# Optimization experiments

Hardware: AMD Instinct MI355X
Metric: run time of the kernel (lower is better)

Reference implementation:

```python
import jax, jax.numpy as jnp
import numpy as np

L, B, T, S, W, H = 4, 2, 2048, 512, 512, 8  # layers, batch, n_ctx, cond units, width, heads
CH = W // H


def _ln(x, g, b):
    m = x.mean(-1, keepdims=True)
    v = ((x - m) ** 2).mean(-1, keepdims=True)
    return (x - m) * jax.lax.rsqrt(v + 1e-5) * g + b


def setup_inputs() -> dict:
    key = jax.random.key(0)
    ks = jax.random.split(key, 16)
    std = 0.25 * np.sqrt(1.0 / W)  # init_scale * sqrt(1/width), as in Transformer.__init__
    f32 = jnp.float32
    d = {
        "x": jax.random.normal(ks[0], (B, T, W), f32),
        "cond_k": jax.random.normal(ks[1], (B, S, W), f32),
        "cond_v": jax.random.normal(ks[2], (B, S, W), f32),
        # stacked per-layer params; weights stored [in, out] (torch Linear transposed)
        "qkv_w": jax.random.normal(ks[3], (L, W, 3 * W), f32) * std,
        "qkv_b": jnp.zeros((L, 3 * W), f32),
        "attn_proj_w": jax.random.normal(ks[4], (L, W, W), f32) * std,
        "attn_proj_b": jnp.zeros((L, W), f32),
        "cross_proj_w": jax.random.normal(ks[5], (L, W, W), f32) * std,
        "cross_proj_b": jnp.zeros((L, W), f32),
        "fc_w": jax.random.normal(ks[6], (L, W, 4 * W), f32) * std,
        "fc_b": jnp.zeros((L, 4 * W), f32),
        "mlp_proj_w": jax.random.normal(ks[7], (L, 4 * W, W), f32) * std,
        "mlp_proj_b": jnp.zeros((L, W), f32),
        "ln1_g": jnp.ones((L, W), f32), "ln1_b": jnp.zeros((L, W), f32),
        "ln3_g": jnp.ones((L, W), f32), "ln3_b": jnp.zeros((L, W), f32),
        "ln4_g": jnp.ones((L, W), f32), "ln4_b": jnp.zeros((L, W), f32),
    }
    return d


def reference(x, cond_k, cond_v, qkv_w, qkv_b, attn_proj_w, attn_proj_b,
              cross_proj_w, cross_proj_b, fc_w, fc_b, mlp_proj_w, mlp_proj_b,
              ln1_g, ln1_b, ln3_g, ln3_b, ln4_g, ln4_b):
    b, t, w = x.shape
    ch = w // H
    scale = 1.0 / np.sqrt(np.sqrt(ch))  # applied to both q and k, as in torch code
    kk = cond_k.reshape(b, -1, H, ch)
    vv = cond_v.reshape(b, -1, H, ch)
    n_layers = qkv_w.shape[0]
    for i in range(n_layers):
        # ---- self-attention ----
        h = _ln(x, ln1_g[i], ln1_b[i])
        qkv = (h @ qkv_w[i] + qkv_b[i]).reshape(b, t, H, 3 * ch)
        q, k, v = qkv[..., :ch], qkv[..., ch:2 * ch], qkv[..., 2 * ch:]
        wts = jnp.einsum('bthc,bshc->bhts', q * scale, k * scale)
        wts = jax.nn.softmax(wts.astype(jnp.float32), axis=-1).astype(wts.dtype)
        a = jnp.einsum('bhts,bshc->bthc', wts, v).reshape(b, t, w)
        x = x + a @ attn_proj_w[i] + attn_proj_b[i]
        # ---- cross-attention (q is ln_3(x) directly, no q projection) ----
        h = _ln(x, ln3_g[i], ln3_b[i])
        q = h.reshape(b, t, H, ch)
        wts = jnp.einsum('bthc,bshc->bhts', q * scale, kk * scale)
        wts = jax.nn.softmax(wts.astype(jnp.float32), axis=-1).astype(wts.dtype)
        a = jnp.einsum('bhts,bshc->bthc', wts, vv).reshape(b, t, w)
        x = x + a @ cross_proj_w[i] + cross_proj_b[i]
        # ---- MLP (exact erf GELU, as torch nn.GELU default) ----
        h = _ln(x, ln4_g[i], ln4_b[i])
        h = jax.nn.gelu(h @ fc_w[i] + fc_b[i], approximate=False)
        x = x + h @ mlp_proj_w[i] + mlp_proj_b[i]
    return x
```

## Files before the change

### kernel.cpp

```cpp
#include <hip/hip_runtime.h>
#include <hip/hip_bf16.h>
#include <cstdint>


typedef __bf16 bf16;
typedef __bf16 bf16x8 __attribute__((ext_vector_type(8)));
typedef float f32x4 __attribute__((ext_vector_type(4)));

#define AS1(p) ((__attribute__((address_space(1))) void*)(uintptr_t)(p))
#define AS3(p) ((__attribute__((address_space(3))) void*)(p))

__device__ __forceinline__ unsigned short bf2us(bf16 v) {
    return __builtin_bit_cast(unsigned short, v);
}

__global__ __launch_bounds__(256) void ln_kernel(const float* __restrict__ x,
                                                 const float* __restrict__ gam,
                                                 const float* __restrict__ bet,
                                                 bf16* __restrict__ h) {
    int row  = blockIdx.x * 4 + (threadIdx.x >> 6);
    int lane = threadIdx.x & 63;
    const float4* xr = (const float4*)(x + (size_t)row * 512) + lane * 2;
    float4 a = xr[0], b = xr[1];
    float s  = a.x + a.y + a.z + a.w + b.x + b.y + b.z + b.w;
    float ss = a.x * a.x + a.y * a.y + a.z * a.z + a.w * a.w +
               b.x * b.x + b.y * b.y + b.z * b.z + b.w * b.w;
#pragma unroll
    for (int off = 1; off < 64; off <<= 1) {
        s  += __shfl_xor(s, off);
        ss += __shfl_xor(ss, off);
    }
    float mean = s * (1.f / 512.f);
    float var  = ss * (1.f / 512.f) - mean * mean;
    float rstd = rsqrtf(fmaxf(var, 0.f) + 1e-5f);
    const float4* gr = (const float4*)gam + lane * 2;
    const float4* br = (const float4*)bet + lane * 2;
    float4 g0 = gr[0], g1 = gr[1], b0 = br[0], b1 = br[1];
    bf16x8 hv;
    hv[0] = (bf16)((a.x - mean) * rstd * g0.x + b0.x);
    hv[1] = (bf16)((a.y - mean) * rstd * g0.y + b0.y);
    hv[2] = (bf16)((a.z - mean) * rstd * g0.z + b0.z);
    hv[3] = (bf16)((a.w - mean) * rstd * g0.w + b0.w);
    hv[4] = (bf16)((b.x - mean) * rstd * g1.x + b1.x);
    hv[5] = (bf16)((b.y - mean) * rstd * g1.y + b1.y);
    hv[6] = (bf16)((b.z - mean) * rstd * g1.z + b1.z);
    hv[7] = (bf16)((b.w - mean) * rstd * g1.w + b1.w);
    *(bf16x8*)(h + (size_t)row * 512 + lane * 8) = hv;
}

__global__ void wtrans_kernel(const float* __restrict__ in, bf16* __restrict__ out,
                              int K, int N) {
    __shared__ float tile[32][33];
    int n0 = blockIdx.x * 32, k0 = blockIdx.y * 32;
    const float* ip = in + (size_t)blockIdx.z * K * N;
    bf16* op = out + (size_t)blockIdx.z * N * K;
#pragma unroll
    for (int i = threadIdx.y; i < 32; i += 8)
        tile[i][threadIdx.x] = ip[(size_t)(k0 + i) * N + n0 + threadIdx.x];
    __syncthreads();
#pragma unroll
    for (int i = threadIdx.y; i < 32; i += 8)
        op[(size_t)(n0 + i) * K + k0 + threadIdx.x] = (bf16)tile[threadIdx.x][i];
}

__global__ void cvt_kernel(const float* __restrict__ in, bf16* __restrict__ out, int n) {
    int i = (blockIdx.x * 256 + threadIdx.x) * 8;
    if (i + 8 <= n) {
        const float4* p = (const float4*)(in + i);
        float4 a = p[0], b = p[1];
        bf16x8 v;
        v[0] = (bf16)a.x; v[1] = (bf16)a.y; v[2] = (bf16)a.z; v[3] = (bf16)a.w;
        v[4] = (bf16)b.x; v[5] = (bf16)b.y; v[6] = (bf16)b.z; v[7] = (bf16)b.w;
        *(bf16x8*)(out + i) = v;
    }
}

__global__ __launch_bounds__(256) void vtrans_self(const bf16* __restrict__ qkvb,
                                                   bf16* __restrict__ VTs, int T_) {
    __shared__ bf16 tl[64][66];
    int tb = blockIdx.x * 64;
    int bh = blockIdx.y;
    int b = bh >> 3, h = bh & 7;
    int tid = threadIdx.x;
#pragma unroll
    for (int e = 0; e < 2; ++e) {
        int idx = e * 256 + tid;
        int t = idx >> 3, ci = (idx & 7) * 8;
        bf16x8 v = *(const bf16x8*)(qkvb + ((size_t)b * T_ + tb + t) * 1536 +
                                    h * 192 + 128 + ci);
#pragma unroll
        for (int j = 0; j < 8; ++j) tl[ci + j][t] = v[j];
    }
    __syncthreads();
#pragma unroll
    for (int e = 0; e < 2; ++e) {
        int idx = e * 256 + tid;
        int ch = idx >> 3, ti = (idx & 7) * 8;
        bf16x8 v;
#pragma unroll
        for (int j = 0; j < 8; ++j) v[j] = tl[ch][ti + j];
        *(bf16x8*)(VTs + ((size_t)bh * 64 + ch) * T_ + tb + ti) = v;
    }
}

__global__ __launch_bounds__(256) void vtrans_cross(const float* __restrict__ cv,
                                                    bf16* __restrict__ VTc, int S_) {
    __shared__ bf16 tl[64][66];
    int sb = blockIdx.x * 64;
    int bh = blockIdx.y;
    int b = bh >> 3, h = bh & 7;
    int tid = threadIdx.x;
#pragma unroll
    for (int e = 0; e < 4; ++e) {
        int idx = e * 256 + tid;
        int s = idx >> 4, ci = (idx & 15) * 4;
        float4 v = *(const float4*)(cv + ((size_t)b * S_ + sb + s) * 512 + h * 64 + ci);
        tl[ci + 0][s] = (bf16)v.x; tl[ci + 1][s] = (bf16)v.y;
        tl[ci + 2][s] = (bf16)v.z; tl[ci + 3][s] = (bf16)v.w;
    }
    __syncthreads();
#pragma unroll
    for (int e = 0; e < 2; ++e) {
        int idx = e * 256 + tid;
        int ch = idx >> 3, si = (idx & 7) * 8;
        bf16x8 v;
#pragma unroll
        for (int j = 0; j < 8; ++j) v[j] = tl[ch][si + j];
        *(bf16x8*)(VTc + ((size_t)bh * 64 + ch) * S_ + sb + si) = v;
    }
}

template <int EPI, int BM>
__global__ __launch_bounds__(256) void gemm_kernel(const bf16* __restrict__ A,
                                                   const bf16* __restrict__ Bt,
                                                   const float* __restrict__ bias,
                                                   const float* res, void* out,
                                                   int M, int N, int K) {
    constexpr int MI = BM / 32;
    __shared__ __align__(16) bf16 As[BM * 64];
    __shared__ __align__(16) bf16 Bs[128 * 64];
    int tiles_n = N >> 7;
    int bid = blockIdx.x;
    int cpx = gridDim.x >> 3;
    bid = (bid & 7) * cpx + (bid >> 3);
    int bm = bid / tiles_n, bn = bid % tiles_n;
    int tid = threadIdx.x, wave = tid >> 6, lane = tid & 63;
    int wm = wave >> 1, wn = wave & 1;
    int g = lane >> 4, cc = lane & 15;
    f32x4 acc[MI][4] = {};
    const bf16* Ag = A + (size_t)(bm * BM) * K;
    const bf16* Bg = Bt + (size_t)(bn << 7) * K;
    int scol = (tid & 7) * 8;

    for (int k0 = 0; k0 < K; k0 += 64) {
        __syncthreads();
#pragma unroll
        for (int e = 0; e < BM / 32; ++e) {
            int row = (e * 256 + tid) >> 3;
            __builtin_amdgcn_global_load_lds(AS1(Ag + (size_t)row * K + k0 + scol),
                                             AS3((char*)As + e * 4096 + wave * 1024), 16, 0, 0);
        }
#pragma unroll
        for (int e = 0; e < 4; ++e) {
            int row = (e * 256 + tid) >> 3;
            __builtin_amdgcn_global_load_lds(AS1(Bg + (size_t)row * K + k0 + scol),
                                             AS3((char*)Bs + e * 4096 + wave * 1024), 16, 0, 0);
        }
        __syncthreads();
#pragma unroll
        for (int kk = 0; kk < 2; ++kk) {
            bf16x8 af[MI], bfr[4];
#pragma unroll
            for (int mi = 0; mi < MI; ++mi)
                af[mi] = *(const bf16x8*)(As + (wm * (BM / 2) + mi * 16 + cc) * 64 + kk * 32 + g * 8);
#pragma unroll
            for (int ni = 0; ni < 4; ++ni)
                bfr[ni] = *(const bf16x8*)(Bs + (wn * 64 + ni * 16 + cc) * 64 + kk * 32 + g * 8);
#pragma unroll
            for (int mi = 0; mi < MI; ++mi)
#pragma unroll
                for (int ni = 0; ni < 4; ++ni)
                    acc[mi][ni] = __builtin_amdgcn_mfma_f32_16x16x32_bf16(
                        af[mi], bfr[ni], acc[mi][ni], 0, 0, 0);
        }
    }
    int m0 = bm * BM + wm * (BM / 2);
    int n0 = (bn << 7) + wn * 64;
#pragma unroll
    for (int ni = 0; ni < 4; ++ni) {
        int n = n0 + ni * 16 + cc;
        float bv = bias[n];
#pragma unroll
        for (int mi = 0; mi < MI; ++mi) {
#pragma unroll
            for (int r = 0; r < 4; ++r) {
                int m = m0 + mi * 16 + g * 4 + r;
                float v = acc[mi][ni][r] + bv;
                if (EPI == 1) v = 0.5f * v * (1.f + erff(v * 0.70710678118654752f));
                if (EPI == 2)
                    ((float*)out)[(size_t)m * N + n] = res[(size_t)m * N + n] + v;
                else
                    ((bf16*)out)[(size_t)m * N + n] = (bf16)v;
            }
        }
    }
}

__global__ __launch_bounds__(256) void attn_kernel(
    const bf16* __restrict__ Qp, int q_rs, int q_hs,
    const bf16* __restrict__ Kp, int k_rs, int k_hs,
    const bf16* __restrict__ Vt, int vt_s,
    bf16* __restrict__ Op, int T_, int S_) {
    __shared__ __align__(16) char KB[2][16384];
    __shared__ __align__(16) char VB[2][16384];
    __shared__ __align__(16) char PB[4][4096];

    int numQ = T_ >> 6;
    int phys = blockIdx.x;
    int cpx = gridDim.x >> 3;
    int bid = (phys & 7) * cpx + (phys >> 3);
    int qb = bid % numQ;
    int bh = bid / numQ;
    int b = bh >> 3, h = bh & 7;
    int tid = threadIdx.x, wave = tid >> 6, lane = tid & 63;
    int g = lane >> 4, cc = lane & 15;
    int xr = cc & 7;
    int qrow0 = qb * 64 + wave * 16;

    const bf16* Qb = Qp + ((size_t)b * T_ + qrow0) * q_rs + h * q_hs;
    const bf16* Kb = Kp + ((size_t)b * S_) * k_rs + h * k_hs;
    const bf16* Vtb = Vt + (size_t)bh * 64 * vt_s;

    const float QSC = 0.125f * 1.44269504088896f;
    bf16x8 q0r = *(const bf16x8*)(Qb + (size_t)cc * q_rs + g * 8);
    bf16x8 q1r = *(const bf16x8*)(Qb + (size_t)cc * q_rs + 32 + g * 8);
    bf16x8 qf0, qf1;
#pragma unroll
    for (int j = 0; j < 8; ++j) {
        qf0[j] = (bf16)((float)q0r[j] * QSC);
        qf1[j] = (bf16)((float)q1r[j] * QSC);
    }

    float l_part = 0.f;
    f32x4 o_acc[4] = {};
    char* Pw = PB[wave];

    auto stage = [&](int s0, int buf) {
#pragma unroll
        for (int e = 0; e < 4; ++e) {
            int L = e * 256 + tid;
            int row = L >> 3, cp = L & 7;
            int col = (cp ^ (row & 7)) * 8;
            __builtin_amdgcn_global_load_lds(AS1(Kb + (size_t)(s0 + row) * k_rs + col),
                                             AS3(KB[buf] + e * 4096 + wave * 1024), 16, 0, 0);
        }
#pragma unroll
        for (int e = 0; e < 4; ++e) {
            int L = e * 256 + tid;
            int row = L >> 4, cp = L & 15;
            int scl = (cp ^ (row & 15)) * 8;
            __builtin_amdgcn_global_load_lds(AS1(Vtb + (size_t)row * vt_s + s0 + scl),
                                             AS3(VB[buf] + e * 4096 + wave * 1024), 16, 0, 0);
        }
    };

    stage(0, 0);
    __syncthreads();

    int nt = S_ >> 7;
    int cur = 0;
    for (int t = 0; t < nt; ++t) {
        if (t + 1 < nt) stage((t + 1) * 128, cur ^ 1);
        f32x4 sf[2][4] = {};
        __builtin_amdgcn_s_setprio(1);
#pragma unroll
        for (int kk = 0; kk < 2; ++kk) {
            int co = ((kk * 4 + g) ^ xr) << 4;
#pragma unroll
            for (int st = 0; st < 2; ++st)
#pragma unroll
                for (int sn = 0; sn < 4; ++sn) {
                    bf16x8 kf = *(const bf16x8*)(KB[cur] + (st * 64 + sn * 16 + cc) * 128 + co);
                    sf[st][sn] = __builtin_amdgcn_mfma_f32_16x16x32_bf16(
                        kf, kk ? qf1 : qf0, sf[st][sn], 0, 0, 0);
                }
        }
        __builtin_amdgcn_s_setprio(0);
#pragma unroll
        for (int st = 0; st < 2; ++st)
#pragma unroll
            for (int sn = 0; sn < 4; ++sn) {
                float p0 = exp2f(sf[st][sn][0]), p1 = exp2f(sf[st][sn][1]);
                float p2 = exp2f(sf[st][sn][2]), p3 = exp2f(sf[st][sn][3]);
                l_part += (p0 + p1) + (p2 + p3);
                uint32_t u01 = (uint32_t)bf2us((bf16)p0) | ((uint32_t)bf2us((bf16)p1) << 16);
                uint32_t u23 = (uint32_t)bf2us((bf16)p2) | ((uint32_t)bf2us((bf16)p3) << 16);
                int chunk = st * 8 + sn * 2 + (g >> 1);
                char* pb = Pw + cc * 256 + ((chunk ^ cc) << 4) + (g & 1) * 8;
                uint2 uu; uu.x = u01; uu.y = u23;
                *(uint2*)pb = uu;
            }
        __builtin_amdgcn_s_setprio(1);
#pragma unroll
        for (int st = 0; st < 2; ++st)
#pragma unroll
            for (int kk = 0; kk < 2; ++kk) {
                int pchunk = st * 8 + kk * 4 + g;
                bf16x8 pa = *(const bf16x8*)(Pw + cc * 256 + ((pchunk ^ cc) << 4));
#pragma unroll
                for (int ni = 0; ni < 4; ++ni) {
                    int vrow = ni * 16 + cc;
                    bf16x8 vf = *(const bf16x8*)(VB[cur] + vrow * 256 + ((pchunk ^ (vrow & 15)) << 4));
                    o_acc[ni] = __builtin_amdgcn_mfma_f32_16x16x32_bf16(
                        pa, vf, o_acc[ni], 0, 0, 0);
                }
            }
        __builtin_amdgcn_s_setprio(0);
        __syncthreads();
        cur ^= 1;
    }

    l_part += __shfl_xor(l_part, 16);
    l_part += __shfl_xor(l_part, 32);
#pragma unroll
    for (int r = 0; r < 4; ++r) {
        float lq = __shfl(l_part, 4 * g + r);
        float inv = 1.f / lq;
#pragma unroll
        for (int ni = 0; ni < 4; ++ni) {
            Op[((size_t)b * T_ + qrow0 + 4 * g + r) * 512 + h * 64 + ni * 16 + cc] =
                (bf16)(o_acc[ni][r] * inv);
        }
    }
}

extern "C" void kernel_launch(void* const* d_in, const int* in_sizes, int n_in,
                              void* d_out, int out_size, void* d_ws, size_t ws_size,
                              hipStream_t stream) {
    const float* x_in    = (const float*)d_in[0];
    const float* cond_k  = (const float*)d_in[1];
    const float* cond_v  = (const float*)d_in[2];
    const float* qkv_w   = (const float*)d_in[3];
    const float* qkv_b   = (const float*)d_in[4];
    const float* attn_w  = (const float*)d_in[5];
    const float* attn_b  = (const float*)d_in[6];
    const float* cross_w = (const float*)d_in[7];
    const float* cross_b = (const float*)d_in[8];
    const float* fc_w    = (const float*)d_in[9];
    const float* fc_b    = (const float*)d_in[10];
    const float* mlp_w   = (const float*)d_in[11];
    const float* mlp_b   = (const float*)d_in[12];
    const float* ln1_g   = (const float*)d_in[13];
    const float* ln1_b   = (const float*)d_in[14];
    const float* ln3_g   = (const float*)d_in[15];
    const float* ln3_b   = (const float*)d_in[16];
    const float* ln4_g   = (const float*)d_in[17];
    const float* ln4_b   = (const float*)d_in[18];

    const int L = 4, T = 2048, S = 512, W = 512;
    const int M = 2 * T;

    char* ws = (char*)d_ws;
    size_t off = 0;
    auto carve = [&](size_t bytes) -> char* {
        char* p = ws + off;
        off += (bytes + 255) & ~(size_t)255;
        return p;
    };
    bf16* wqkv  = (bf16*)carve((size_t)L * 1536 * 512 * 2);
    bf16* wattn = (bf16*)carve((size_t)L * 512 * 512 * 2);
    bf16* wcrs  = (bf16*)carve((size_t)L * 512 * 512 * 2);
    bf16* wfc   = (bf16*)carve((size_t)L * 2048 * 512 * 2);
    bf16* wmlp  = (bf16*)carve((size_t)L * 512 * 2048 * 2);
    bf16* ckb   = (bf16*)carve((size_t)2 * S * W * 2);
    bf16* VTs   = (bf16*)carve((size_t)16 * 64 * T * 2);
    bf16* VTc   = (bf16*)carve((size_t)16 * 64 * S * 2);
    bf16* hbuf  = (bf16*)carve((size_t)M * 512 * 2);
    bf16* qkvb  = (bf16*)carve((size_t)M * 1536 * 2);
    bf16* abuf  = (bf16*)carve((size_t)M * 512 * 2);
    bf16* fcb   = (bf16*)carve((size_t)M * 2048 * 2);

    dim3 tb(32, 8);
    wtrans_kernel<<<dim3(1536 / 32, 512 / 32, L), tb, 0, stream>>>(qkv_w, wqkv, 512, 1536);
    wtrans_kernel<<<dim3(512 / 32, 512 / 32, L), tb, 0, stream>>>(attn_w, wattn, 512, 512);
    wtrans_kernel<<<dim3(512 / 32, 512 / 32, L), tb, 0, stream>>>(cross_w, wcrs, 512, 512);
    wtrans_kernel<<<dim3(2048 / 32, 512 / 32, L), tb, 0, stream>>>(fc_w, wfc, 512, 2048);
    wtrans_kernel<<<dim3(512 / 32, 2048 / 32, L), tb, 0, stream>>>(mlp_w, wmlp, 2048, 512);
    cvt_kernel<<<(2 * S * W) / 2048, 256, 0, stream>>>(cond_k, ckb, 2 * S * W);
    vtrans_cross<<<dim3(S / 64, 16), 256, 0, stream>>>(cond_v, VTc, S);

    float* x = (float*)d_out;
    hipMemcpyAsync(x, (const void*)x_in, (size_t)M * W * sizeof(float),
                   hipMemcpyDeviceToDevice, stream);

    const int nAttn = 16 * (T / 64);
    for (int i = 0; i < L; ++i) {
        ln_kernel<<<M / 4, 256, 0, stream>>>(x, ln1_g + i * 512, ln1_b + i * 512, hbuf);
        gemm_kernel<0, 64><<<(M / 64) * (1536 / 128), 256, 0, stream>>>(
            hbuf, wqkv + (size_t)i * 1536 * 512, qkv_b + i * 1536, nullptr, qkvb,
            M, 1536, 512);
        vtrans_self<<<dim3(T / 64, 16), 256, 0, stream>>>(qkvb, VTs, T);
        attn_kernel<<<nAttn, 256, 0, stream>>>(
            qkvb, 1536, 192, qkvb + 64, 1536, 192, VTs, T,
            abuf, T, T);
        gemm_kernel<2, 64><<<(M / 64) * (512 / 128), 256, 0, stream>>>(
            abuf, wattn + (size_t)i * 512 * 512, attn_b + i * 512, x, x,
            M, 512, 512);
        ln_kernel<<<M / 4, 256, 0, stream>>>(x, ln3_g + i * 512, ln3_b + i * 512, hbuf);
        attn_kernel<<<nAttn, 256, 0, stream>>>(
            hbuf, 512, 64, ckb, 512, 64, VTc, S,
            abuf, T, S);
        gemm_kernel<2, 64><<<(M / 64) * (512 / 128), 256, 0, stream>>>(
            abuf, wcrs + (size_t)i * 512 * 512, cross_b + i * 512, x, x,
            M, 512, 512);
        ln_kernel<<<M / 4, 256, 0, stream>>>(x, ln4_g + i * 512, ln4_b + i * 512, hbuf);
        gemm_kernel<1, 128><<<(M / 128) * (2048 / 128), 256, 0, stream>>>(
            hbuf, wfc + (size_t)i * 2048 * 512, fc_b + i * 2048, nullptr, fcb,
            M, 2048, 512);
        gemm_kernel<2, 64><<<(M / 64) * (512 / 128), 256, 0, stream>>>(
            fcb, wmlp + (size_t)i * 512 * 2048, mlp_b + i * 512, x, x,
            M, 512, 2048);
    }
}
```

Baseline: 726.6 us.

## Split attention keys across waves with LDS reduction; shrink residual GEMM tiles

The attention kernel now gives each wave all 64 query rows of the block and a 32-key slice of each 128-key tile, instead of 16 query rows over all keys. Each K and V fragment loaded from LDS therefore feeds four query sub-tiles, cutting LDS read traffic per MFMA. The per-wave partial outputs and row sums are then combined through LDS at the end, and the result is written with vectorized stores. This adds an extra sync plus reduction, and raises register pressure from the 4x4 accumulators. Separately, the N=512 residual GEMMs use 32-row tiles to launch twice as many blocks, trading per-block reuse for more parallelism.

```diff
diff --git a/kernel.cpp b/kernel.cpp
--- a/kernel.cpp
+++ b/kernel.cpp
@@ -136,7 +136,7 @@
                                                    const float* __restrict__ bias,
                                                    const float* res, void* out,
                                                    int M, int N, int K) {
-    constexpr int MI = BM / 32;
+    constexpr int MI = (BM + 31) / 32;
     __shared__ __align__(16) bf16 As[BM * 64];
     __shared__ __align__(16) bf16 Bs[128 * 64];
     int tiles_n = N >> 7;
@@ -211,9 +211,7 @@
     const bf16* __restrict__ Kp, int k_rs, int k_hs,
     const bf16* __restrict__ Vt, int vt_s,
     bf16* __restrict__ Op, int T_, int S_) {
-    __shared__ __align__(16) char KB[2][16384];
-    __shared__ __align__(16) char VB[2][16384];
-    __shared__ __align__(16) char PB[4][4096];
+    __shared__ __align__(16) char SM[81920];
 
     int numQ = T_ >> 6;
     int phys = blockIdx.x;
@@ -224,35 +222,40 @@
     int b = bh >> 3, h = bh & 7;
     int tid = threadIdx.x, wave = tid >> 6, lane = tid & 63;
     int g = lane >> 4, cc = lane & 15;
-    int xr = cc & 7;
-    int qrow0 = qb * 64 + wave * 16;
+    int qrow0 = qb * 64;
+    int sw = wave * 32;
 
     const bf16* Qb = Qp + ((size_t)b * T_ + qrow0) * q_rs + h * q_hs;
     const bf16* Kb = Kp + ((size_t)b * S_) * k_rs + h * k_hs;
     const bf16* Vtb = Vt + (size_t)bh * 64 * vt_s;
 
     const float QSC = 0.125f * 1.44269504088896f;
-    bf16x8 q0r = *(const bf16x8*)(Qb + (size_t)cc * q_rs + g * 8);
-    bf16x8 q1r = *(const bf16x8*)(Qb + (size_t)cc * q_rs + 32 + g * 8);
-    bf16x8 qf0, qf1;
-#pragma unroll
-    for (int j = 0; j < 8; ++j) {
-        qf0[j] = (bf16)((float)q0r[j] * QSC);
-        qf1[j] = (bf16)((float)q1r[j] * QSC);
-    }
-
-    float l_part = 0.f;
-    f32x4 o_acc[4] = {};
-    char* Pw = PB[wave];
+    bf16x8 qf[4][2];
+#pragma unroll
+    for (int qn = 0; qn < 4; ++qn)
+#pragma unroll
+        for (int kk = 0; kk < 2; ++kk) {
+            bf16x8 raw = *(const bf16x8*)(Qb + (size_t)(qn * 16 + cc) * q_rs + kk * 32 + g * 8);
+            bf16x8 sc;
+#pragma unroll
+            for (int j = 0; j < 8; ++j) sc[j] = (bf16)((float)raw[j] * QSC);
+            qf[qn][kk] = sc;
+        }
+
+    float l_acc[4] = {0.f, 0.f, 0.f, 0.f};
+    f32x4 o_acc[4][4] = {};
+    char* Pw = SM + 65536 + wave * 4096;
 
     auto stage = [&](int s0, int buf) {
+        char* kb = SM + buf * 16384;
+        char* vb = SM + 32768 + buf * 16384;
 #pragma unroll
         for (int e = 0; e < 4; ++e) {
             int L = e * 256 + tid;
             int row = L >> 3, cp = L & 7;
             int col = (cp ^ (row & 7)) * 8;
             __builtin_amdgcn_global_load_lds(AS1(Kb + (size_t)(s0 + row) * k_rs + col),
-                                             AS3(KB[buf] + e * 4096 + wave * 1024), 16, 0, 0);
+                                             AS3(kb + e * 4096 + wave * 1024), 16, 0, 0);
         }
 #pragma unroll
         for (int e = 0; e < 4; ++e) {
@@ -260,7 +263,7 @@
             int row = L >> 4, cp = L & 15;
             int scl = (cp ^ (row & 15)) * 8;
             __builtin_amdgcn_global_load_lds(AS1(Vtb + (size_t)row * vt_s + s0 + scl),
-                                             AS3(VB[buf] + e * 4096 + wave * 1024), 16, 0, 0);
+                                             AS3(vb + e * 4096 + wave * 1024), 16, 0, 0);
         }
     };
 
@@ -271,67 +274,97 @@
     int cur = 0;
     for (int t = 0; t < nt; ++t) {
         if (t + 1 < nt) stage((t + 1) * 128, cur ^ 1);
+        char* kbc = SM + cur * 16384;
+        char* vbc = SM + 32768 + cur * 16384;
         f32x4 sf[2][4] = {};
         __builtin_amdgcn_s_setprio(1);
 #pragma unroll
-        for (int kk = 0; kk < 2; ++kk) {
-            int co = ((kk * 4 + g) ^ xr) << 4;
-#pragma unroll
-            for (int st = 0; st < 2; ++st)
-#pragma unroll
-                for (int sn = 0; sn < 4; ++sn) {
-                    bf16x8 kf = *(const bf16x8*)(KB[cur] + (st * 64 + sn * 16 + cc) * 128 + co);
-                    sf[st][sn] = __builtin_amdgcn_mfma_f32_16x16x32_bf16(
-                        kf, kk ? qf1 : qf0, sf[st][sn], 0, 0, 0);
-                }
-        }
+        for (int kk = 0; kk < 2; ++kk)
+#pragma unroll
+            for (int sn = 0; sn < 2; ++sn) {
+                int row = sw + sn * 16 + cc;
+                bf16x8 kf = *(const bf16x8*)(kbc + row * 128 + (((kk * 4 + g) ^ (cc & 7)) << 4));
+#pragma unroll
+                for (int qn = 0; qn < 4; ++qn)
+                    sf[sn][qn] = __builtin_amdgcn_mfma_f32_16x16x32_bf16(
+                        kf, qf[qn][kk], sf[sn][qn], 0, 0, 0);
+            }
         __builtin_amdgcn_s_setprio(0);
 #pragma unroll
-        for (int st = 0; st < 2; ++st)
-#pragma unroll
-            for (int sn = 0; sn < 4; ++sn) {
-                float p0 = exp2f(sf[st][sn][0]), p1 = exp2f(sf[st][sn][1]);
-                float p2 = exp2f(sf[st][sn][2]), p3 = exp2f(sf[st][sn][3]);
-                l_part += (p0 + p1) + (p2 + p3);
+        for (int sn = 0; sn < 2; ++sn)
+#pragma unroll
+            for (int qn = 0; qn < 4; ++qn) {
+                float p0 = exp2f(sf[sn][qn][0]), p1 = exp2f(sf[sn][qn][1]);
+                float p2 = exp2f(sf[sn][qn][2]), p3 = exp2f(sf[sn][qn][3]);
+                l_acc[qn] += (p0 + p1) + (p2 + p3);
                 uint32_t u01 = (uint32_t)bf2us((bf16)p0) | ((uint32_t)bf2us((bf16)p1) << 16);
                 uint32_t u23 = (uint32_t)bf2us((bf16)p2) | ((uint32_t)bf2us((bf16)p3) << 16);
-                int chunk = st * 8 + sn * 2 + (g >> 1);
-                char* pb = Pw + cc * 256 + ((chunk ^ cc) << 4) + (g & 1) * 8;
+                int chunk = sn * 2 + (g >> 1);
+                char* pb = Pw + (qn * 16 + cc) * 64 + (((chunk ^ (cc & 3))) << 4) + (g & 1) * 8;
                 uint2 uu; uu.x = u01; uu.y = u23;
                 *(uint2*)pb = uu;
             }
         __builtin_amdgcn_s_setprio(1);
-#pragma unroll
-        for (int st = 0; st < 2; ++st)
-#pragma unroll
-            for (int kk = 0; kk < 2; ++kk) {
-                int pchunk = st * 8 + kk * 4 + g;
-                bf16x8 pa = *(const bf16x8*)(Pw + cc * 256 + ((pchunk ^ cc) << 4));
-#pragma unroll
-                for (int ni = 0; ni < 4; ++ni) {
-                    int vrow = ni * 16 + cc;
-                    bf16x8 vf = *(const bf16x8*)(VB[cur] + vrow * 256 + ((pchunk ^ (vrow & 15)) << 4));
-                    o_acc[ni] = __builtin_amdgcn_mfma_f32_16x16x32_bf16(
-                        pa, vf, o_acc[ni], 0, 0, 0);
-                }
-            }
+        bf16x8 pa[4], vf[4];
+#pragma unroll
+        for (int qn = 0; qn < 4; ++qn)
+            pa[qn] = *(const bf16x8*)(Pw + (qn * 16 + cc) * 64 + ((g ^ (cc & 3)) << 4));
+#pragma unroll
+        for (int ni = 0; ni < 4; ++ni)
+            vf[ni] = *(const bf16x8*)(vbc + (ni * 16 + cc) * 256 + (((wave * 4 + g) ^ cc) << 4));
+#pragma unroll
+        for (int qn = 0; qn < 4; ++qn)
+#pragma unroll
+            for (int ni = 0; ni < 4; ++ni)
+                o_acc[qn][ni] = __builtin_amdgcn_mfma_f32_16x16x32_bf16(
+                    pa[qn], vf[ni], o_acc[qn][ni], 0, 0, 0);
         __builtin_amdgcn_s_setprio(0);
         __syncthreads();
         cur ^= 1;
     }
 
-    l_part += __shfl_xor(l_part, 16);
-    l_part += __shfl_xor(l_part, 32);
-#pragma unroll
-    for (int r = 0; r < 4; ++r) {
-        float lq = __shfl(l_part, 4 * g + r);
-        float inv = 1.f / lq;
-#pragma unroll
-        for (int ni = 0; ni < 4; ++ni) {
-            Op[((size_t)b * T_ + qrow0 + 4 * g + r) * 512 + h * 64 + ni * 16 + cc] =
-                (bf16)(o_acc[ni][r] * inv);
-        }
-    }
+#pragma unroll
+    for (int qn = 0; qn < 4; ++qn) {
+        l_acc[qn] += __shfl_xor(l_acc[qn], 16);
+        l_acc[qn] += __shfl_xor(l_acc[qn], 32);
+    }
+    float* sc = (float*)SM;
+    float* lf = (float*)(SM + 65536);
+#pragma unroll
+    for (int qn = 0; qn < 4; ++qn)
+#pragma unroll
+        for (int ni = 0; ni < 4; ++ni)
+#pragma unroll
+            for (int r = 0; r < 4; ++r)
+                sc[wave * 4096 + (qn * 16 + 4 * g + r) * 64 + ni * 16 + cc] = o_acc[qn][ni][r];
+    if (g == 0) {
+#pragma unroll
+        for (int qn = 0; qn < 4; ++qn) lf[wave * 64 + qn * 16 + cc] = l_acc[qn];
+    }
+    __syncthreads();
+    int q = tid >> 2, c0 = (tid & 3) * 16;
+    float l = lf[q] + lf[64 + q] + lf[128 + q] + lf[192 + q];
+    float inv = 1.f / l;
+    float acc[16] = {};
+#pragma unroll
+    for (int w = 0; w < 4; ++w) {
+        const float* p = sc + w * 4096 + q * 64 + c0;
+#pragma unroll
+        for (int e = 0; e < 4; ++e) {
+            float4 v = *(const float4*)(p + e * 4);
+            acc[e * 4 + 0] += v.x; acc[e * 4 + 1] += v.y;
+            acc[e * 4 + 2] += v.z; acc[e * 4 + 3] += v.w;
+        }
+    }
+    bf16x8 o1, o2;
+#pragma unroll
+    for (int j = 0; j < 8; ++j) {
+        o1[j] = (bf16)(acc[j] * inv);
+        o2[j] = (bf16)(acc[8 + j] * inv);
+    }
+    bf16* dst = Op + ((size_t)b * T_ + qrow0 + q) * 512 + h * 64 + c0;
+    *(bf16x8*)dst = o1;
+    *(bf16x8*)(dst + 8) = o2;
 }
 
 extern "C" void kernel_launch(void* const* d_in, const int* in_sizes, int n_in,
@@ -403,21 +436,21 @@
         attn_kernel<<<nAttn, 256, 0, stream>>>(
             qkvb, 1536, 192, qkvb + 64, 1536, 192, VTs, T,
             abuf, T, T);
-        gemm_kernel<2, 64><<<(M / 64) * (512 / 128), 256, 0, stream>>>(
+        gemm_kernel<2, 32><<<(M / 32) * (512 / 128), 256, 0, stream>>>(
             abuf, wattn + (size_t)i * 512 * 512, attn_b + i * 512, x, x,
             M, 512, 512);
         ln_kernel<<<M / 4, 256, 0, stream>>>(x, ln3_g + i * 512, ln3_b + i * 512, hbuf);
         attn_kernel<<<nAttn, 256, 0, stream>>>(
             hbuf, 512, 64, ckb, 512, 64, VTc, S,
             abuf, T, S);
-        gemm_kernel<2, 64><<<(M / 64) * (512 / 128), 256, 0, stream>>>(
+        gemm_kernel<2, 32><<<(M / 32) * (512 / 128), 256, 0, stream>>>(
             abuf, wcrs + (size_t)i * 512 * 512, cross_b + i * 512, x, x,
             M, 512, 512);
         ln_kernel<<<M / 4, 256, 0, stream>>>(x, ln4_g + i * 512, ln4_b + i * 512, hbuf);
         gemm_kernel<1, 128><<<(M / 128) * (2048 / 128), 256, 0, stream>>>(
             hbuf, wfc + (size_t)i * 2048 * 512, fc_b + i * 2048, nullptr, fcb,
             M, 2048, 512);
-        gemm_kernel<2, 64><<<(M / 64) * (512 / 128), 256, 0, stream>>>(
+        gemm_kernel<2, 32><<<(M / 32) * (512 / 128), 256, 0, stream>>>(
             fcb, wmlp + (size_t)i * 512 * 2048, mlp_b + i * 512, x, x,
             M, 512, 2048);
     }
```

Result: faster. 687.2 us (-5.4%).

## Split attention key range across wave pairs and shrink residual GEMM tiles

Applied to the files above, without the earlier changes.

The attention kernel now runs 512 threads per block. Each pair of waves shares a 16-row query strip and splits each 64-key tile between them. Partial outputs and row sums are combined through shared memory at the end, and the result is written with vector stores. The key tile shrinks from 128 to 64 with smaller LDS buffers, and the residual-add GEMMs use BM=32 tiles to launch more blocks. The goal is more parallelism and occupancy for these launches, at the cost of an extra cross-wave reduction, more barriers per key, and less data reuse per GEMM block.

```diff
diff --git a/kernel.cpp b/kernel.cpp
--- a/kernel.cpp
+++ b/kernel.cpp
@@ -136,7 +136,7 @@
                                                    const float* __restrict__ bias,
                                                    const float* res, void* out,
                                                    int M, int N, int K) {
-    constexpr int MI = BM / 32;
+    constexpr int MI = (BM + 31) / 32;
     __shared__ __align__(16) bf16 As[BM * 64];
     __shared__ __align__(16) bf16 Bs[128 * 64];
     int tiles_n = N >> 7;
@@ -206,14 +206,12 @@
     }
 }
 
-__global__ __launch_bounds__(256) void attn_kernel(
+__global__ __launch_bounds__(512) void attn_kernel(
     const bf16* __restrict__ Qp, int q_rs, int q_hs,
     const bf16* __restrict__ Kp, int k_rs, int k_hs,
     const bf16* __restrict__ Vt, int vt_s,
     bf16* __restrict__ Op, int T_, int S_) {
-    __shared__ __align__(16) char KB[2][16384];
-    __shared__ __align__(16) char VB[2][16384];
-    __shared__ __align__(16) char PB[4][4096];
+    __shared__ __align__(16) char SM[40960];
 
     int numQ = T_ >> 6;
     int phys = blockIdx.x;
@@ -223,115 +221,112 @@
     int bh = bid / numQ;
     int b = bh >> 3, h = bh & 7;
     int tid = threadIdx.x, wave = tid >> 6, lane = tid & 63;
+    int wq = wave >> 1, ws = wave & 1;
     int g = lane >> 4, cc = lane & 15;
-    int xr = cc & 7;
-    int qrow0 = qb * 64 + wave * 16;
-
-    const bf16* Qb = Qp + ((size_t)b * T_ + qrow0) * q_rs + h * q_hs;
+    int qrow0 = qb * 64;
+    int swz = (cc >> 1) & 3;
+
+    const bf16* Qb = Qp + ((size_t)b * T_ + qrow0 + wq * 16) * q_rs + h * q_hs;
     const bf16* Kb = Kp + ((size_t)b * S_) * k_rs + h * k_hs;
     const bf16* Vtb = Vt + (size_t)bh * 64 * vt_s;
 
     const float QSC = 0.125f * 1.44269504088896f;
-    bf16x8 q0r = *(const bf16x8*)(Qb + (size_t)cc * q_rs + g * 8);
-    bf16x8 q1r = *(const bf16x8*)(Qb + (size_t)cc * q_rs + 32 + g * 8);
-    bf16x8 qf0, qf1;
-#pragma unroll
-    for (int j = 0; j < 8; ++j) {
-        qf0[j] = (bf16)((float)q0r[j] * QSC);
-        qf1[j] = (bf16)((float)q1r[j] * QSC);
-    }
-
-    float l_part = 0.f;
+    bf16x8 qf[2];
+#pragma unroll
+    for (int kk = 0; kk < 2; ++kk) {
+        bf16x8 raw = *(const bf16x8*)(Qb + (size_t)cc * q_rs + kk * 32 + g * 8);
+        bf16x8 sc;
+#pragma unroll
+        for (int j = 0; j < 8; ++j) sc[j] = (bf16)((float)raw[j] * QSC);
+        qf[kk] = sc;
+    }
+
+    float l_acc = 0.f;
     f32x4 o_acc[4] = {};
-    char* Pw = PB[wave];
+    char* Pw = SM + 32768 + wave * 1024;
 
     auto stage = [&](int s0, int buf) {
-#pragma unroll
-        for (int e = 0; e < 4; ++e) {
-            int L = e * 256 + tid;
-            int row = L >> 3, cp = L & 7;
-            int col = (cp ^ (row & 7)) * 8;
-            __builtin_amdgcn_global_load_lds(AS1(Kb + (size_t)(s0 + row) * k_rs + col),
-                                             AS3(KB[buf] + e * 4096 + wave * 1024), 16, 0, 0);
-        }
-#pragma unroll
-        for (int e = 0; e < 4; ++e) {
-            int L = e * 256 + tid;
-            int row = L >> 4, cp = L & 15;
-            int scl = (cp ^ (row & 15)) * 8;
-            __builtin_amdgcn_global_load_lds(AS1(Vtb + (size_t)row * vt_s + s0 + scl),
-                                             AS3(VB[buf] + e * 4096 + wave * 1024), 16, 0, 0);
-        }
+        int row = tid >> 3, cp = tid & 7;
+        int col = (cp ^ (row & 7)) * 8;
+        __builtin_amdgcn_global_load_lds(AS1(Kb + (size_t)(s0 + row) * k_rs + col),
+                                         AS3(SM + buf * 8192 + wave * 1024), 16, 0, 0);
+        __builtin_amdgcn_global_load_lds(AS1(Vtb + (size_t)row * vt_s + s0 + col),
+                                         AS3(SM + 16384 + buf * 8192 + wave * 1024), 16, 0, 0);
     };
 
     stage(0, 0);
     __syncthreads();
 
-    int nt = S_ >> 7;
+    int nt = S_ >> 6;
     int cur = 0;
     for (int t = 0; t < nt; ++t) {
-        if (t + 1 < nt) stage((t + 1) * 128, cur ^ 1);
-        f32x4 sf[2][4] = {};
+        if (t + 1 < nt) stage((t + 1) * 64, cur ^ 1);
+        char* kbc = SM + cur * 8192;
+        char* vbc = SM + 16384 + cur * 8192;
+        f32x4 sf[2] = {};
         __builtin_amdgcn_s_setprio(1);
 #pragma unroll
-        for (int kk = 0; kk < 2; ++kk) {
-            int co = ((kk * 4 + g) ^ xr) << 4;
-#pragma unroll
-            for (int st = 0; st < 2; ++st)
-#pragma unroll
-                for (int sn = 0; sn < 4; ++sn) {
-                    bf16x8 kf = *(const bf16x8*)(KB[cur] + (st * 64 + sn * 16 + cc) * 128 + co);
-                    sf[st][sn] = __builtin_amdgcn_mfma_f32_16x16x32_bf16(
-                        kf, kk ? qf1 : qf0, sf[st][sn], 0, 0, 0);
-                }
-        }
+        for (int kk = 0; kk < 2; ++kk)
+#pragma unroll
+            for (int sn = 0; sn < 2; ++sn) {
+                int row = ws * 32 + sn * 16 + cc;
+                bf16x8 kf = *(const bf16x8*)(kbc + row * 128 + (((kk * 4 + g) ^ (cc & 7)) << 4));
+                sf[sn] = __builtin_amdgcn_mfma_f32_16x16x32_bf16(kf, qf[kk], sf[sn], 0, 0, 0);
+            }
         __builtin_amdgcn_s_setprio(0);
 #pragma unroll
-        for (int st = 0; st < 2; ++st)
-#pragma unroll
-            for (int sn = 0; sn < 4; ++sn) {
-                float p0 = exp2f(sf[st][sn][0]), p1 = exp2f(sf[st][sn][1]);
-                float p2 = exp2f(sf[st][sn][2]), p3 = exp2f(sf[st][sn][3]);
-                l_part += (p0 + p1) + (p2 + p3);
-                uint32_t u01 = (uint32_t)bf2us((bf16)p0) | ((uint32_t)bf2us((bf16)p1) << 16);
-                uint32_t u23 = (uint32_t)bf2us((bf16)p2) | ((uint32_t)bf2us((bf16)p3) << 16);
-                int chunk = st * 8 + sn * 2 + (g >> 1);
-                char* pb = Pw + cc * 256 + ((chunk ^ cc) << 4) + (g & 1) * 8;
-                uint2 uu; uu.x = u01; uu.y = u23;
-                *(uint2*)pb = uu;
-            }
+        for (int sn = 0; sn < 2; ++sn) {
+            float p0 = exp2f(sf[sn][0]), p1 = exp2f(sf[sn][1]);
+            float p2 = exp2f(sf[sn][2]), p3 = exp2f(sf[sn][3]);
+            l_acc += (p0 + p1) + (p2 + p3);
+            uint32_t u01 = (uint32_t)bf2us((bf16)p0) | ((uint32_t)bf2us((bf16)p1) << 16);
+            uint32_t u23 = (uint32_t)bf2us((bf16)p2) | ((uint32_t)bf2us((bf16)p3) << 16);
+            char* pb = Pw + cc * 64 + (((sn * 2 + (g >> 1)) ^ swz) << 4) + (g & 1) * 8;
+            uint2 uu; uu.x = u01; uu.y = u23;
+            *(uint2*)pb = uu;
+        }
         __builtin_amdgcn_s_setprio(1);
-#pragma unroll
-        for (int st = 0; st < 2; ++st)
-#pragma unroll
-            for (int kk = 0; kk < 2; ++kk) {
-                int pchunk = st * 8 + kk * 4 + g;
-                bf16x8 pa = *(const bf16x8*)(Pw + cc * 256 + ((pchunk ^ cc) << 4));
-#pragma unroll
-                for (int ni = 0; ni < 4; ++ni) {
-                    int vrow = ni * 16 + cc;
-                    bf16x8 vf = *(const bf16x8*)(VB[cur] + vrow * 256 + ((pchunk ^ (vrow & 15)) << 4));
-                    o_acc[ni] = __builtin_amdgcn_mfma_f32_16x16x32_bf16(
-                        pa, vf, o_acc[ni], 0, 0, 0);
-                }
-            }
+        bf16x8 pa = *(const bf16x8*)(Pw + cc * 64 + ((g ^ swz) << 4));
+#pragma unroll
+        for (int ni = 0; ni < 4; ++ni) {
+            int vrow = ni * 16 + cc;
+            bf16x8 vf = *(const bf16x8*)(vbc + vrow * 128 + (((ws * 4 + g) ^ (cc & 7)) << 4));
+            o_acc[ni] = __builtin_amdgcn_mfma_f32_16x16x32_bf16(pa, vf, o_acc[ni], 0, 0, 0);
+        }
         __builtin_amdgcn_s_setprio(0);
         __syncthreads();
         cur ^= 1;
     }
 
-    l_part += __shfl_xor(l_part, 16);
-    l_part += __shfl_xor(l_part, 32);
-#pragma unroll
-    for (int r = 0; r < 4; ++r) {
-        float lq = __shfl(l_part, 4 * g + r);
-        float inv = 1.f / lq;
-#pragma unroll
-        for (int ni = 0; ni < 4; ++ni) {
-            Op[((size_t)b * T_ + qrow0 + 4 * g + r) * 512 + h * 64 + ni * 16 + cc] =
-                (bf16)(o_acc[ni][r] * inv);
-        }
-    }
+    l_acc += __shfl_xor(l_acc, 16);
+    l_acc += __shfl_xor(l_acc, 32);
+    float* sco = (float*)SM;
+    float* lf = (float*)(SM + 32768);
+    float* scw = sco + wave * 1024;
+#pragma unroll
+    for (int ni = 0; ni < 4; ++ni)
+#pragma unroll
+        for (int r = 0; r < 4; ++r)
+            scw[(4 * g + r) * 64 + ni * 16 + cc] = o_acc[ni][r];
+    if (g == 0) lf[wave * 16 + cc] = l_acc;
+    __syncthreads();
+    int q = tid >> 3, c0 = (tid & 7) * 8;
+    int wqq = q >> 4, qr = q & 15;
+    float l = lf[(wqq * 2) * 16 + qr] + lf[(wqq * 2 + 1) * 16 + qr];
+    float inv = 1.f / l;
+    const float* p0p = sco + (wqq * 2) * 1024 + qr * 64 + c0;
+    const float* p1p = sco + (wqq * 2 + 1) * 1024 + qr * 64 + c0;
+    bf16x8 o1;
+#pragma unroll
+    for (int e = 0; e < 2; ++e) {
+        float4 v0 = *(const float4*)(p0p + e * 4);
+        float4 v1 = *(const float4*)(p1p + e * 4);
+        o1[e * 4 + 0] = (bf16)((v0.x + v1.x) * inv);
+        o1[e * 4 + 1] = (bf16)((v0.y + v1.y) * inv);
+        o1[e * 4 + 2] = (bf16)((v0.z + v1.z) * inv);
+        o1[e * 4 + 3] = (bf16)((v0.w + v1.w) * inv);
+    }
+    *(bf16x8*)(Op + ((size_t)b * T_ + qrow0 + q) * 512 + h * 64 + c0) = o1;
 }
 
 extern "C" void kernel_launch(void* const* d_in, const int* in_sizes, int n_in,
@@ -400,24 +395,24 @@
             hbuf, wqkv + (size_t)i * 1536 * 512, qkv_b + i * 1536, nullptr, qkvb,
             M, 1536, 512);
         vtrans_self<<<dim3(T / 64, 16), 256, 0, stream>>>(qkvb, VTs, T);
-        attn_kernel<<<nAttn, 256, 0, stream>>>(
+        attn_kernel<<<nAttn, 512, 0, stream>>>(
             qkvb, 1536, 192, qkvb + 64, 1536, 192, VTs, T,
             abuf, T, T);
-        gemm_kernel<2, 64><<<(M / 64) * (512 / 128), 256, 0, stream>>>(
+        gemm_kernel<2, 32><<<(M / 32) * (512 / 128), 256, 0, stream>>>(
             abuf, wattn + (size_t)i * 512 * 512, attn_b + i * 512, x, x,
             M, 512, 512);
         ln_kernel<<<M / 4, 256, 0, stream>>>(x, ln3_g + i * 512, ln3_b + i * 512, hbuf);
-        attn_kernel<<<nAttn, 256, 0, stream>>>(
+        attn_kernel<<<nAttn, 512, 0, stream>>>(
             hbuf, 512, 64, ckb, 512, 64, VTc, S,
             abuf, T, S);
-        gemm_kernel<2, 64><<<(M / 64) * (512 / 128), 256, 0, stream>>>(
+        gemm_kernel<2, 32><<<(M / 32) * (512 / 128), 256, 0, stream>>>(
             abuf, wcrs + (size_t)i * 512 * 512, cross_b + i * 512, x, x,
             M, 512, 512);
         ln_kernel<<<M / 4, 256, 0, stream>>>(x, ln4_g + i * 512, ln4_b + i * 512, hbuf);
         gemm_kernel<1, 128><<<(M / 128) * (2048 / 128), 256, 0, stream>>>(
             hbuf, wfc + (size_t)i * 2048 * 512, fc_b + i * 2048, nullptr, fcb,
             M, 2048, 512);
-        gemm_kernel<2, 64><<<(M / 64) * (512 / 128), 256, 0, stream>>>(
+        gemm_kernel<2, 32><<<(M / 32) * (512 / 128), 256, 0, stream>>>(
             fcb, wmlp + (size_t)i * 512 * 2048, mlp_b + i * 512, x, x,
             M, 512, 2048);
     }
```

Result: faster. 654.5 us (-9.9%).
